# Optimization experiments

Measured on AMD Instinct MI355X. Metric: run time of the kernel, lower is better.

Reference implementation:

```python
import jax, jax.numpy as jnp
import numpy as np

P, H_OUT, D, NX = 32, 1, 256, 16
S_A = -0.1

def layernorm(x, g, b, eps=1e-5):
    mu = jnp.mean(x, axis=-1, keepdims=True)
    var = jnp.var(x, axis=-1, keepdims=True)
    return (x - mu) * jax.lax.rsqrt(var + eps) * g + b

def setup_inputs() -> dict:
    key = jax.random.key(0)
    ks = jax.random.split(key, 16)
    B, L = 8, 2048
    y = jax.random.normal(ks[0], (B, L, P), jnp.float32)
    Win = jax.random.normal(ks[1], (P, D), jnp.float32) / np.sqrt(P)
    bin_ = jnp.zeros((D,), jnp.float32)
    ng = jnp.ones((D,), jnp.float32); nb = jnp.zeros((D,), jnp.float32)
    # A = -10*rand + s_A, with A[:,0] = s_A (fix first state of each channel)
    A = -10.0 * jax.random.uniform(ks[2], (D, NX), jnp.float32) + S_A
    A = A.at[:, 0].set(S_A)
    W_B = jax.random.normal(ks[3], (NX, D), jnp.float32)
    W_C = jax.random.normal(ks[4], (NX, D), jnp.float32)
    q_delta = jax.random.normal(ks[5], (D,), jnp.float32)
    p_delta = jax.random.normal(ks[6], (1,), jnp.float32)
    nfg = jnp.ones((D,), jnp.float32); nfb = jnp.zeros((D,), jnp.float32)
    W1 = jax.random.normal(ks[7], (D, D), jnp.float32) / np.sqrt(D)
    b1 = jnp.zeros((D,), jnp.float32)
    W2 = jax.random.normal(ks[8], (D, H_OUT * P), jnp.float32) / np.sqrt(D)
    b2 = jnp.zeros((H_OUT * P,), jnp.float32)
    return {"y": y, "Win": Win, "bin_": bin_, "ng": ng, "nb": nb, "A": A,
            "W_B": W_B, "W_C": W_C, "q_delta": q_delta, "p_delta": p_delta,
            "nfg": nfg, "nfb": nfb, "W1": W1, "b1": b1, "W2": W2, "b2": b2}

def selective_scan(u, delta, A, Bm, Cm):
    # u: (B,L,D), delta: (B,L), A: (D,NX), Bm/Cm: (B,L,NX)
    dA = jnp.exp(delta[..., None, None] * A)                      # (B,L,D,NX)
    dBu = delta[..., None, None] * Bm[:, :, None, :] * u[..., None]  # (B,L,D,NX)
    x0 = jnp.zeros((u.shape[0], u.shape[2], A.shape[1]), u.dtype)
    def step(x, inp):
        dA_t, dBu_t, C_t = inp
        x = dA_t * x + dBu_t                                      # (B,D,NX)
        y_t = jnp.einsum('bdn,bn->bd', x, C_t)
        return x, y_t
    _, ys = jax.lax.scan(step, x0, (dA.transpose(1, 0, 2, 3),
                                    dBu.transpose(1, 0, 2, 3),
                                    Cm.transpose(1, 0, 2)))
    return ys.transpose(1, 0, 2)                                  # (B,L,D)

def reference(y, Win, bin_, ng, nb, A, W_B, W_C, q_delta, p_delta,
              nfg, nfb, W1, b1, W2, b2):
    B, L, _ = y.shape
    h = y @ Win + bin_                                            # (B,L,D)
    hn = layernorm(h, ng, nb)
    delta = jax.nn.softplus(p_delta[0] + jnp.einsum('bld,d->bl', hn, q_delta))
    Bm = jnp.einsum('nd,bld->bln', W_B, hn)
    Cm = jnp.einsum('nd,bld->bln', W_C, hn)
    upd = selective_scan(hn, delta, A, Bm, Cm)
    h = h + upd
    h = layernorm(h, nfg, nfb)
    out = jax.nn.gelu(h @ W1 + b1, approximate=False) @ W2 + b2
    return out.reshape(B, L, H_OUT, P)
```

## Files before the change

### kernel.cpp

```cpp
#include <hip/hip_runtime.h>
#include <math.h>

#define D 256
#define NX 16
#define L 2048
#define NBATCH 8
#define NTOK (NBATCH * L)
#define CL 32
#define NCH (L / CL)
#define LOG2E 1.44269504088896340736f

typedef float f32x4 __attribute__((ext_vector_type(4)));
typedef short bf16x8 __attribute__((ext_vector_type(8)));

__device__ __forceinline__ unsigned short f2bf(float x) {
  unsigned u = __float_as_uint(x);
  u = u + 0x7fffu + ((u >> 16) & 1u);
  return (unsigned short)(u >> 16);
}
__device__ __forceinline__ float bf2f(unsigned short h) {
  return __uint_as_float(((unsigned)h) << 16);
}

__global__ __launch_bounds__(256) void k0_prep(const float* __restrict__ A,
                                               const float* __restrict__ WB,
                                               const float* __restrict__ WC,
                                               const float* __restrict__ W1,
                                               const float* __restrict__ W2,
                                               float* __restrict__ At,
                                               float* __restrict__ Wbct,
                                               unsigned short* __restrict__ W1fh,
                                               unsigned short* __restrict__ W1fl,
                                               unsigned short* __restrict__ W2fh,
                                               unsigned short* __restrict__ W2fl) {
  int i = blockIdx.x * 256 + threadIdx.x;
  if (i < 4096) {
    int d = i >> 4, n = i & 15;
    At[n * D + d] = A[i] * LOG2E;
  } else if (i < 12288) {
    int j = i - 4096;
    int d = j >> 5, c = j & 31;
    Wbct[j] = (c < 16) ? WB[c * D + d] : WC[(c - 16) * D + d];
  } else if (i < 77824) {
    int e = i - 12288;
    int j = e & 7, l = (e >> 3) & 63, tt = (e >> 9) & 15, s = e >> 13;
    int k = s * 32 + ((l >> 4) << 3) + j;
    int n = tt * 16 + (l & 15);
    float x = W1[k * 256 + n];
    unsigned short h = f2bf(x);
    W1fh[e] = h;
    W1fl[e] = f2bf(x - bf2f(h));
  } else {
    int e = i - 77824;
    int j = e & 7, l = (e >> 3) & 63, tt = (e >> 9) & 1, s = e >> 10;
    int k = s * 32 + ((l >> 4) << 3) + j;
    int n = tt * 16 + (l & 15);
    float x = W2[k * 32 + n];
    unsigned short h = f2bf(x);
    W2fh[e] = h;
    W2fl[e] = f2bf(x - bf2f(h));
  }
}

__global__ __launch_bounds__(256) void k1a_front_scan(
    const float* __restrict__ y, const float* __restrict__ Win,
    const float* __restrict__ bin_, const float* __restrict__ ng,
    const float* __restrict__ nb, const float* __restrict__ Wbct,
    const float* __restrict__ qd, const float* __restrict__ pd,
    const float* __restrict__ At,
    float* __restrict__ hn, float* __restrict__ delta,
    float* __restrict__ Bm, float* __restrict__ Cm,
    float* __restrict__ muv, float* __restrict__ irsv,
    float* __restrict__ EX, float* __restrict__ T) {
  __shared__ float sy[32][32];
  __shared__ float sh[32][260];
  __shared__ float sB[32][NX];
  __shared__ float sdelta[32];
  int t = threadIdx.x;
  int tok0 = blockIdx.x * 32;
  {
    const float4* src = (const float4*)(y + (size_t)tok0 * 32);
    ((float4*)sy)[t] = src[t];
  }
  __syncthreads();
  int dcol = t & 63;
  int jrow = t >> 6;
  int d4 = dcol * 4;
  float4 bv = ((const float4*)bin_)[dcol];
  float4 acc[8];
  #pragma unroll
  for (int jj = 0; jj < 8; ++jj) acc[jj] = bv;
  const float4* Win4 = (const float4*)Win;
  #pragma unroll
  for (int k = 0; k < 32; ++k) {
    float4 wv = Win4[k * 64 + dcol];
    #pragma unroll
    for (int jj = 0; jj < 8; ++jj) {
      float av = sy[jrow * 8 + jj][k];
      acc[jj].x = fmaf(av, wv.x, acc[jj].x);
      acc[jj].y = fmaf(av, wv.y, acc[jj].y);
      acc[jj].z = fmaf(av, wv.z, acc[jj].z);
      acc[jj].w = fmaf(av, wv.w, acc[jj].w);
    }
  }
  float4 g4 = ((const float4*)ng)[dcol];
  float4 nb4 = ((const float4*)nb)[dcol];
  float4 q4 = ((const float4*)qd)[dcol];
  float pd0 = pd[0];
  #pragma unroll
  for (int jj = 0; jj < 8; ++jj) {
    int j = jrow * 8 + jj;
    int tok = tok0 + j;
    float4 a = acc[jj];
    float s1 = a.x + a.y + a.z + a.w;
    float s2 = a.x * a.x + a.y * a.y + a.z * a.z + a.w * a.w;
    #pragma unroll
    for (int off = 1; off < 64; off <<= 1) {
      s1 += __shfl_xor(s1, off);
      s2 += __shfl_xor(s2, off);
    }
    float mu = s1 * (1.f / D);
    float var = s2 * (1.f / D) - mu * mu;
    float rstd = rsqrtf(var + 1e-5f);
    if (dcol == 0) { muv[tok] = mu; irsv[tok] = sqrtf(var + 1e-5f); }
    float4 v4;
    v4.x = (a.x - mu) * rstd * g4.x + nb4.x;
    v4.y = (a.y - mu) * rstd * g4.y + nb4.y;
    v4.z = (a.z - mu) * rstd * g4.z + nb4.z;
    v4.w = (a.w - mu) * rstd * g4.w + nb4.w;
    ((float4*)(hn + (size_t)tok * D))[dcol] = v4;
    *(float4*)&sh[j][d4] = v4;
    float dd = v4.x * q4.x + v4.y * q4.y + v4.z * q4.z + v4.w * q4.w;
    #pragma unroll
    for (int off = 1; off < 64; off <<= 1) dd += __shfl_xor(dd, off);
    if (dcol == 0) {
      float xx = pd0 + dd;
      float dv = (xx > 20.f) ? xx : log1pf(expf(xx));
      delta[tok] = dv;
      sdelta[j] = dv;
    }
  }
  __syncthreads();
  if (t < 32) {
    float v = sdelta[t];
    #pragma unroll
    for (int off = 1; off < 32; off <<= 1) v += __shfl_xor(v, off);
    if (t == 0) T[blockIdx.x] = v;
  }
  int col4 = t & 7;
  int j = t >> 3;
  const float4* W4 = (const float4*)Wbct;
  float4 o = make_float4(0.f, 0.f, 0.f, 0.f);
  #pragma unroll 8
  for (int d = 0; d < 256; ++d) {
    float av = sh[j][d];
    float4 w = W4[d * 8 + col4];
    o.x = fmaf(av, w.x, o.x);
    o.y = fmaf(av, w.y, o.y);
    o.z = fmaf(av, w.z, o.z);
    o.w = fmaf(av, w.w, o.w);
  }
  int tokj = tok0 + j;
  if (col4 < 4) {
    ((float4*)(Bm + (size_t)tokj * NX))[col4] = o;
    *(float4*)&sB[j][col4 * 4] = o;
  } else {
    ((float4*)(Cm + (size_t)tokj * NX))[col4 - 4] = o;
  }
  __syncthreads();
  float a16[16];
  #pragma unroll
  for (int n = 0; n < 16; ++n) a16[n] = At[n * D + t];
  float x16[16];
  #pragma unroll
  for (int n = 0; n < 16; ++n) x16[n] = 0.f;
  for (int lo = 0; lo < CL; ++lo) {
    float dlt = sdelta[lo];
    float du = dlt * sh[lo][t];
    #pragma unroll
    for (int n = 0; n < 16; ++n)
      x16[n] = fmaf(exp2f(dlt * a16[n]), x16[n], du * sB[lo][n]);
  }
  size_t exbase = (size_t)blockIdx.x * (NX * D) + t;
  #pragma unroll
  for (int n = 0; n < 16; ++n) EX[exbase + n * D] = x16[n];
}

__global__ __launch_bounds__(256) void k2b_chunkscan(
    const float* __restrict__ At, const float* __restrict__ T,
    float* __restrict__ EX) {
  __shared__ float sT[NCH];
  int b = blockIdx.x >> 4;
  int rem = ((blockIdx.x & 15) << 8) | threadIdx.x;
  if (threadIdx.x < NCH) sT[threadIdx.x] = T[b * NCH + threadIdx.x];
  __syncthreads();
  float A2 = At[rem];
  size_t base = ((size_t)b << 18) + rem;
  float eq[4];
  #pragma unroll
  for (int j = 0; j < 4; ++j) eq[j] = EX[base + ((size_t)j << 12)];
  float x = 0.f;
  #pragma unroll 4
  for (int c = 0; c < NCH; ++c) {
    float e = eq[c & 3];
    if (c + 4 < NCH) eq[c & 3] = EX[base + ((size_t)(c + 4) << 12)];
    EX[base + ((size_t)c << 12)] = x;
    x = fmaf(exp2f(sT[c] * A2), x, e);
  }
}

__device__ __forceinline__ float gelu_exact(float x) {
  return 0.5f * x * (1.f + erff(x * 0.70710678118654752440f));
}

__global__ __launch_bounds__(256) void k2cd_scan_mlp(
    const float* __restrict__ hn, const float* __restrict__ delta,
    const float* __restrict__ Bm, const float* __restrict__ Cm,
    const float* __restrict__ At, const float* __restrict__ EX,
    const float* __restrict__ muv, const float* __restrict__ irsv,
    const float* __restrict__ ng, const float* __restrict__ nb,
    const float* __restrict__ nfg, const float* __restrict__ nfb,
    const unsigned short* __restrict__ W1fh, const unsigned short* __restrict__ W1fl,
    const unsigned short* __restrict__ W2fh, const unsigned short* __restrict__ W2fl,
    const float* __restrict__ b1, const float* __restrict__ b2,
    float* __restrict__ out) {
  __shared__ float s_az[32 * 260];
  __shared__ __align__(16) unsigned short sAh[32 * 256];
  __shared__ __align__(16) unsigned short sAl[32 * 256];
  __shared__ float sB[32][NX];
  __shared__ float sC[32][NX];
  __shared__ float sdelta[32];
  __shared__ float smu[32];
  __shared__ float sirs[32];
  int t = threadIdx.x;
  int tok0 = blockIdx.x * 32;
  size_t tokbase = (size_t)tok0;
  if (t < 32) {
    sdelta[t] = delta[tokbase + t];
    smu[t] = muv[tokbase + t];
    sirs[t] = irsv[tokbase + t];
  }
  for (int i = t; i < 32 * NX; i += 256) {
    ((float*)sB)[i] = Bm[tokbase * NX + i];
    ((float*)sC)[i] = Cm[tokbase * NX + i];
  }
  float a16[16], x16[16];
  size_t exbase = (size_t)blockIdx.x * (NX * D) + t;
  #pragma unroll
  for (int n = 0; n < 16; ++n) {
    a16[n] = At[n * D + t];
    x16[n] = EX[exbase + n * D];
  }
  float nb_d = nb[t];
  float invg = 1.0f / ng[t];
  __syncthreads();
  for (int lo = 0; lo < CL; ++lo) {
    float hv = hn[(tokbase + lo) * D + t];
    float dlt = sdelta[lo];
    float du = dlt * hv;
    float p = 0.f;
    #pragma unroll
    for (int n = 0; n < 16; ++n) {
      x16[n] = fmaf(exp2f(dlt * a16[n]), x16[n], du * sB[lo][n]);
      p = fmaf(x16[n], sC[lo][n], p);
    }
    float h = fmaf((hv - nb_d) * invg, sirs[lo], smu[lo]);
    s_az[lo * 260 + t] = h + p;
  }
  __syncthreads();
  int dcol = t & 63, jrow = t >> 6;
  int d4 = dcol * 4, j8 = jrow * 8;
  {
    float4 g4 = ((const float4*)nfg)[dcol];
    float4 b4 = ((const float4*)nfb)[dcol];
    for (int jj = 0; jj < 8; ++jj) {
      int lo = j8 + jj;
      float4 v = *(float4*)&s_az[lo * 260 + d4];
      float s1 = v.x + v.y + v.z + v.w;
      float s2 = v.x * v.x + v.y * v.y + v.z * v.z + v.w * v.w;
      #pragma unroll
      for (int off = 1; off < 64; off <<= 1) {
        s1 += __shfl_xor(s1, off);
        s2 += __shfl_xor(s2, off);
      }
      float mu2 = s1 * (1.f / D);
      float var2 = s2 * (1.f / D) - mu2 * mu2;
      float rstd2 = rsqrtf(var2 + 1e-5f);
      float4 o;
      o.x = (v.x - mu2) * rstd2 * g4.x + b4.x;
      o.y = (v.y - mu2) * rstd2 * g4.y + b4.y;
      o.z = (v.z - mu2) * rstd2 * g4.z + b4.z;
      o.w = (v.w - mu2) * rstd2 * g4.w + b4.w;
      unsigned short h0 = f2bf(o.x), h1 = f2bf(o.y), h2 = f2bf(o.z), h3 = f2bf(o.w);
      unsigned short q0 = f2bf(o.x - bf2f(h0));
      unsigned short q1 = f2bf(o.y - bf2f(h1));
      unsigned short q2 = f2bf(o.z - bf2f(h2));
      unsigned short q3 = f2bf(o.w - bf2f(h3));
      unsigned off16 = ((unsigned)(d4 * 2)) ^ ((unsigned)(lo & 7) << 4);
      uint2 hv2, lv2;
      hv2.x = (unsigned)h0 | ((unsigned)h1 << 16);
      hv2.y = (unsigned)h2 | ((unsigned)h3 << 16);
      lv2.x = (unsigned)q0 | ((unsigned)q1 << 16);
      lv2.y = (unsigned)q2 | ((unsigned)q3 << 16);
      *(uint2*)((char*)sAh + lo * 512 + off16) = hv2;
      *(uint2*)((char*)sAl + lo * 512 + off16) = lv2;
    }
  }
  __syncthreads();
  int l = t & 63, w = t >> 6;
  const bf16x8* B1h = (const bf16x8*)W1fh;
  const bf16x8* B1l = (const bf16x8*)W1fl;
  f32x4 acc[2][4];
  #pragma unroll
  for (int m = 0; m < 2; ++m)
    #pragma unroll
    for (int n = 0; n < 4; ++n) {
      f32x4 z4 = {0.f, 0.f, 0.f, 0.f};
      acc[m][n] = z4;
    }
  #pragma unroll 2
  for (int s = 0; s < 8; ++s) {
    bf16x8 ah[2], al[2];
    #pragma unroll
    for (int m = 0; m < 2; ++m) {
      int row = m * 16 + (l & 15);
      unsigned off16 = ((unsigned)(s * 64 + ((l >> 4) << 4))) ^ ((unsigned)(row & 7) << 4);
      ah[m] = *(const bf16x8*)((const char*)sAh + row * 512 + off16);
      al[m] = *(const bf16x8*)((const char*)sAl + row * 512 + off16);
    }
    #pragma unroll
    for (int n = 0; n < 4; ++n) {
      int bi = (s * 16 + w * 4 + n) * 64 + l;
      bf16x8 bh = B1h[bi];
      bf16x8 bl = B1l[bi];
      #pragma unroll
      for (int m = 0; m < 2; ++m) {
        acc[m][n] = __builtin_amdgcn_mfma_f32_16x16x32_bf16(ah[m], bh, acc[m][n], 0, 0, 0);
        acc[m][n] = __builtin_amdgcn_mfma_f32_16x16x32_bf16(al[m], bh, acc[m][n], 0, 0, 0);
        acc[m][n] = __builtin_amdgcn_mfma_f32_16x16x32_bf16(ah[m], bl, acc[m][n], 0, 0, 0);
      }
    }
  }
  __syncthreads();
  #pragma unroll
  for (int n = 0; n < 4; ++n) {
    int colz = w * 64 + n * 16 + (l & 15);
    float b1v = b1[colz];
    #pragma unroll
    for (int m = 0; m < 2; ++m) {
      #pragma unroll
      for (int r = 0; r < 4; ++r) {
        int row = m * 16 + ((l >> 4) << 2) + r;
        float zv = gelu_exact(acc[m][n][r] + b1v);
        unsigned short zh = f2bf(zv);
        unsigned short zl = f2bf(zv - bf2f(zh));
        unsigned off16 = ((unsigned)(colz * 2)) ^ ((unsigned)(row & 7) << 4);
        *(unsigned short*)((char*)sAh + row * 512 + off16) = zh;
        *(unsigned short*)((char*)sAl + row * 512 + off16) = zl;
      }
    }
  }
  __syncthreads();
  int mw = w >> 1, nw = w & 1;
  const bf16x8* B2h = (const bf16x8*)W2fh;
  const bf16x8* B2l = (const bf16x8*)W2fl;
  f32x4 acc2 = {0.f, 0.f, 0.f, 0.f};
  #pragma unroll 2
  for (int s = 0; s < 8; ++s) {
    int row = mw * 16 + (l & 15);
    unsigned off16 = ((unsigned)(s * 64 + ((l >> 4) << 4))) ^ ((unsigned)(row & 7) << 4);
    bf16x8 zh8 = *(const bf16x8*)((const char*)sAh + row * 512 + off16);
    bf16x8 zl8 = *(const bf16x8*)((const char*)sAl + row * 512 + off16);
    int bi = (s * 2 + nw) * 64 + l;
    bf16x8 bh = B2h[bi];
    bf16x8 bl = B2l[bi];
    acc2 = __builtin_amdgcn_mfma_f32_16x16x32_bf16(zh8, bh, acc2, 0, 0, 0);
    acc2 = __builtin_amdgcn_mfma_f32_16x16x32_bf16(zl8, bh, acc2, 0, 0, 0);
    acc2 = __builtin_amdgcn_mfma_f32_16x16x32_bf16(zh8, bl, acc2, 0, 0, 0);
  }
  int colo = nw * 16 + (l & 15);
  float b2v = b2[colo];
  #pragma unroll
  for (int r = 0; r < 4; ++r) {
    int row = mw * 16 + ((l >> 4) << 2) + r;
    out[(size_t)(tok0 + row) * 32 + colo] = acc2[r] + b2v;
  }
}

extern "C" void kernel_launch(void* const* d_in, const int* in_sizes, int n_in,
                              void* d_out, int out_size, void* d_ws, size_t ws_size,
                              hipStream_t stream) {
  const float* y    = (const float*)d_in[0];
  const float* Win  = (const float*)d_in[1];
  const float* bin_ = (const float*)d_in[2];
  const float* ng   = (const float*)d_in[3];
  const float* nb   = (const float*)d_in[4];
  const float* A    = (const float*)d_in[5];
  const float* WB   = (const float*)d_in[6];
  const float* WC   = (const float*)d_in[7];
  const float* qd   = (const float*)d_in[8];
  const float* pd   = (const float*)d_in[9];
  const float* nfg  = (const float*)d_in[10];
  const float* nfb  = (const float*)d_in[11];
  const float* W1   = (const float*)d_in[12];
  const float* b1   = (const float*)d_in[13];
  const float* W2   = (const float*)d_in[14];
  const float* b2   = (const float*)d_in[15];

  float* ws = (float*)d_ws;
  float* hnbuf = ws;
  float* delta = ws + 4194304;
  float* Bm    = delta + NTOK;
  float* Cm    = Bm + NTOK * NX;
  float* muv   = Cm + NTOK * NX;
  float* irsv  = muv + NTOK;
  float* Tbuf  = irsv + NTOK;
  float* At    = Tbuf + NBATCH * NCH;
  float* Wbct  = At + D * NX;
  float* EX    = Wbct + D * 32;
  unsigned short* W1fh = (unsigned short*)(EX + 2097152);
  unsigned short* W1fl = W1fh + 65536;
  unsigned short* W2fh = W1fl + 65536;
  unsigned short* W2fl = W2fh + 8192;

  k0_prep<<<336, 256, 0, stream>>>(A, WB, WC, W1, W2, At, Wbct,
                                   W1fh, W1fl, W2fh, W2fl);
  k1a_front_scan<<<NTOK / 32, 256, 0, stream>>>(y, Win, bin_, ng, nb, Wbct,
                                                qd, pd, At, hnbuf, delta, Bm,
                                                Cm, muv, irsv, EX, Tbuf);
  k2b_chunkscan<<<NBATCH * 16, 256, 0, stream>>>(At, Tbuf, EX);
  k2cd_scan_mlp<<<NTOK / 32, 256, 0, stream>>>(hnbuf, delta, Bm, Cm, At, EX,
                                               muv, irsv, ng, nb, nfg, nfb,
                                               W1fh, W1fl, W2fh, W2fl,
                                               b1, b2, (float*)d_out);
}
```

Baseline: 218.5 us.

## Split front kernel from chunk scan, halve token tile, widen chunkscan grid, add lo*lo MFMA

Splits the fused front/scan kernel in two. The front kernel now uses 16-token blocks and computes the B/C projection as a split-K over two half-warps groups with a shared-memory reduction. A separate scan kernel reloads hn, Bm and delta to build the chunk states. The chunk-prefix kernel moves to 64-thread blocks with a 4x larger grid for more parallelism. The MLP MFMAs also gain a fourth lo*lo product term for accuracy, which adds tensor-core work and extra global traffic from the new kernel launch.

```diff
diff --git a/kernel.cpp b/kernel.cpp
--- a/kernel.cpp
+++ b/kernel.cpp
@@ -62,41 +62,36 @@
   }
 }
 
-__global__ __launch_bounds__(256) void k1a_front_scan(
+__global__ __launch_bounds__(256, 4) void k1a_front(
     const float* __restrict__ y, const float* __restrict__ Win,
     const float* __restrict__ bin_, const float* __restrict__ ng,
     const float* __restrict__ nb, const float* __restrict__ Wbct,
     const float* __restrict__ qd, const float* __restrict__ pd,
-    const float* __restrict__ At,
     float* __restrict__ hn, float* __restrict__ delta,
     float* __restrict__ Bm, float* __restrict__ Cm,
-    float* __restrict__ muv, float* __restrict__ irsv,
-    float* __restrict__ EX, float* __restrict__ T) {
-  __shared__ float sy[32][32];
-  __shared__ float sh[32][260];
-  __shared__ float sB[32][NX];
-  __shared__ float sdelta[32];
+    float* __restrict__ muv, float* __restrict__ irsv) {
+  __shared__ float sy[16][32];
+  __shared__ float sh[16][260];
+  __shared__ float sph[2 * 16 * 32];
   int t = threadIdx.x;
-  int tok0 = blockIdx.x * 32;
-  {
-    const float4* src = (const float4*)(y + (size_t)tok0 * 32);
-    ((float4*)sy)[t] = src[t];
-  }
+  int tok0 = blockIdx.x * 16;
+  if (t < 128)
+    ((float4*)sy)[t] = ((const float4*)(y + (size_t)tok0 * 32))[t];
   __syncthreads();
   int dcol = t & 63;
-  int jrow = t >> 6;
+  int w = t >> 6;
   int d4 = dcol * 4;
   float4 bv = ((const float4*)bin_)[dcol];
-  float4 acc[8];
-  #pragma unroll
-  for (int jj = 0; jj < 8; ++jj) acc[jj] = bv;
+  float4 acc[4];
+  #pragma unroll
+  for (int jj = 0; jj < 4; ++jj) acc[jj] = bv;
   const float4* Win4 = (const float4*)Win;
   #pragma unroll
   for (int k = 0; k < 32; ++k) {
     float4 wv = Win4[k * 64 + dcol];
     #pragma unroll
-    for (int jj = 0; jj < 8; ++jj) {
-      float av = sy[jrow * 8 + jj][k];
+    for (int jj = 0; jj < 4; ++jj) {
+      float av = sy[w * 4 + jj][k];
       acc[jj].x = fmaf(av, wv.x, acc[jj].x);
       acc[jj].y = fmaf(av, wv.y, acc[jj].y);
       acc[jj].z = fmaf(av, wv.z, acc[jj].z);
@@ -108,8 +103,8 @@
   float4 q4 = ((const float4*)qd)[dcol];
   float pd0 = pd[0];
   #pragma unroll
-  for (int jj = 0; jj < 8; ++jj) {
-    int j = jrow * 8 + jj;
+  for (int jj = 0; jj < 4; ++jj) {
+    int j = w * 4 + jj;
     int tok = tok0 + j;
     float4 a = acc[jj];
     float s1 = a.x + a.y + a.z + a.w;
@@ -135,11 +130,57 @@
     for (int off = 1; off < 64; off <<= 1) dd += __shfl_xor(dd, off);
     if (dcol == 0) {
       float xx = pd0 + dd;
-      float dv = (xx > 20.f) ? xx : log1pf(expf(xx));
-      delta[tok] = dv;
-      sdelta[j] = dv;
-    }
-  }
+      delta[tok] = (xx > 20.f) ? xx : log1pf(expf(xx));
+    }
+  }
+  __syncthreads();
+  int c4 = t & 7;
+  int jc = (t >> 3) & 15;
+  int hk = t >> 7;
+  const float* shrow = &sh[jc][hk * 128];
+  const float4* W4 = (const float4*)Wbct + (size_t)hk * 128 * 8;
+  float4 o = make_float4(0.f, 0.f, 0.f, 0.f);
+  #pragma unroll 8
+  for (int k = 0; k < 128; ++k) {
+    float av = shrow[k];
+    float4 wv = W4[k * 8 + c4];
+    o.x = fmaf(av, wv.x, o.x);
+    o.y = fmaf(av, wv.y, o.y);
+    o.z = fmaf(av, wv.z, o.z);
+    o.w = fmaf(av, wv.w, o.w);
+  }
+  *(float4*)&sph[(((hk << 4) | jc) << 5) + c4 * 4] = o;
+  __syncthreads();
+  if (t < 128) {
+    int j2 = t >> 3, cc = t & 7;
+    float4 r0 = *(float4*)&sph[(j2 << 5) + cc * 4];
+    float4 r1 = *(float4*)&sph[((16 + j2) << 5) + cc * 4];
+    float4 r;
+    r.x = r0.x + r1.x; r.y = r0.y + r1.y;
+    r.z = r0.z + r1.z; r.w = r0.w + r1.w;
+    int tokj = tok0 + j2;
+    if (cc < 4) ((float4*)(Bm + (size_t)tokj * NX))[cc] = r;
+    else        ((float4*)(Cm + (size_t)tokj * NX))[cc - 4] = r;
+  }
+}
+
+__global__ __launch_bounds__(256) void k1s_scan(
+    const float* __restrict__ hn, const float* __restrict__ delta,
+    const float* __restrict__ Bm, const float* __restrict__ At,
+    float* __restrict__ EX, float* __restrict__ T) {
+  __shared__ float sh[32][260];
+  __shared__ float sB[32][NX];
+  __shared__ float sdelta[32];
+  int t = threadIdx.x;
+  int tok0 = blockIdx.x * 32;
+  const float4* hn4 = (const float4*)(hn + (size_t)tok0 * D);
+  for (int i = t; i < 2048; i += 256) {
+    int row = i >> 6, c4 = i & 63;
+    *(float4*)&sh[row][c4 * 4] = hn4[i];
+  }
+  for (int i = t; i < 32 * NX; i += 256)
+    ((float*)sB)[i] = Bm[(size_t)tok0 * NX + i];
+  if (t < 32) sdelta[t] = delta[tok0 + t];
   __syncthreads();
   if (t < 32) {
     float v = sdelta[t];
@@ -147,27 +188,6 @@
     for (int off = 1; off < 32; off <<= 1) v += __shfl_xor(v, off);
     if (t == 0) T[blockIdx.x] = v;
   }
-  int col4 = t & 7;
-  int j = t >> 3;
-  const float4* W4 = (const float4*)Wbct;
-  float4 o = make_float4(0.f, 0.f, 0.f, 0.f);
-  #pragma unroll 8
-  for (int d = 0; d < 256; ++d) {
-    float av = sh[j][d];
-    float4 w = W4[d * 8 + col4];
-    o.x = fmaf(av, w.x, o.x);
-    o.y = fmaf(av, w.y, o.y);
-    o.z = fmaf(av, w.z, o.z);
-    o.w = fmaf(av, w.w, o.w);
-  }
-  int tokj = tok0 + j;
-  if (col4 < 4) {
-    ((float4*)(Bm + (size_t)tokj * NX))[col4] = o;
-    *(float4*)&sB[j][col4 * 4] = o;
-  } else {
-    ((float4*)(Cm + (size_t)tokj * NX))[col4 - 4] = o;
-  }
-  __syncthreads();
   float a16[16];
   #pragma unroll
   for (int n = 0; n < 16; ++n) a16[n] = At[n * D + t];
@@ -186,13 +206,13 @@
   for (int n = 0; n < 16; ++n) EX[exbase + n * D] = x16[n];
 }
 
-__global__ __launch_bounds__(256) void k2b_chunkscan(
+__global__ __launch_bounds__(64) void k2b_chunkscan(
     const float* __restrict__ At, const float* __restrict__ T,
     float* __restrict__ EX) {
   __shared__ float sT[NCH];
-  int b = blockIdx.x >> 4;
-  int rem = ((blockIdx.x & 15) << 8) | threadIdx.x;
-  if (threadIdx.x < NCH) sT[threadIdx.x] = T[b * NCH + threadIdx.x];
+  int b = blockIdx.x >> 6;
+  int rem = ((blockIdx.x & 63) << 6) | threadIdx.x;
+  sT[threadIdx.x] = T[b * NCH + threadIdx.x];
   __syncthreads();
   float A2 = At[rem];
   size_t base = ((size_t)b << 18) + rem;
@@ -338,6 +358,7 @@
         acc[m][n] = __builtin_amdgcn_mfma_f32_16x16x32_bf16(ah[m], bh, acc[m][n], 0, 0, 0);
         acc[m][n] = __builtin_amdgcn_mfma_f32_16x16x32_bf16(al[m], bh, acc[m][n], 0, 0, 0);
         acc[m][n] = __builtin_amdgcn_mfma_f32_16x16x32_bf16(ah[m], bl, acc[m][n], 0, 0, 0);
+        acc[m][n] = __builtin_amdgcn_mfma_f32_16x16x32_bf16(al[m], bl, acc[m][n], 0, 0, 0);
       }
     }
   }
@@ -377,6 +398,7 @@
     acc2 = __builtin_amdgcn_mfma_f32_16x16x32_bf16(zh8, bh, acc2, 0, 0, 0);
     acc2 = __builtin_amdgcn_mfma_f32_16x16x32_bf16(zl8, bh, acc2, 0, 0, 0);
     acc2 = __builtin_amdgcn_mfma_f32_16x16x32_bf16(zh8, bl, acc2, 0, 0, 0);
+    acc2 = __builtin_amdgcn_mfma_f32_16x16x32_bf16(zl8, bl, acc2, 0, 0, 0);
   }
   int colo = nw * 16 + (l & 15);
   float b2v = b2[colo];
@@ -425,10 +447,11 @@
 
   k0_prep<<<336, 256, 0, stream>>>(A, WB, WC, W1, W2, At, Wbct,
                                    W1fh, W1fl, W2fh, W2fl);
-  k1a_front_scan<<<NTOK / 32, 256, 0, stream>>>(y, Win, bin_, ng, nb, Wbct,
-                                                qd, pd, At, hnbuf, delta, Bm,
-                                                Cm, muv, irsv, EX, Tbuf);
-  k2b_chunkscan<<<NBATCH * 16, 256, 0, stream>>>(At, Tbuf, EX);
+  k1a_front<<<NTOK / 16, 256, 0, stream>>>(y, Win, bin_, ng, nb, Wbct,
+                                           qd, pd, hnbuf, delta, Bm, Cm,
+                                           muv, irsv);
+  k1s_scan<<<NTOK / 32, 256, 0, stream>>>(hnbuf, delta, Bm, At, EX, Tbuf);
+  k2b_chunkscan<<<NBATCH * 64, 64, 0, stream>>>(At, Tbuf, EX);
   k2cd_scan_mlp<<<NTOK / 32, 256, 0, stream>>>(hnbuf, delta, Bm, Cm, At, EX,
                                                muv, irsv, ng, nb, nfg, nfb,
                                                W1fh, W1fl, W2fh, W2fl,
```

Result: slower. 291.2 us (+33.3%).

## Cut front-kernel register pressure, widen chunk-scan grid, add fourth split-bf16 MFMA term

Applied to the files above, without the earlier changes.

The front kernel now computes its input projection in groups of two tokens rather than holding eight float4 accumulators, and declares launch bounds with a minimum of 4 blocks per multiprocessor, so it needs fewer registers and can keep more waves resident. The chunk-scan kernel is relaunched with 64-thread blocks and four times as many blocks, giving more parallelism across the GPU. The MLP MFMA loops gain a lo×lo product term, which improves precision at the cost of a third more matrix instructions. The grouped loop also reloads the Win weights four times instead of once.

```diff
diff --git a/kernel.cpp b/kernel.cpp
--- a/kernel.cpp
+++ b/kernel.cpp
@@ -62,7 +62,7 @@
   }
 }
 
-__global__ __launch_bounds__(256) void k1a_front_scan(
+__global__ __launch_bounds__(256, 4) void k1a_front_scan(
     const float* __restrict__ y, const float* __restrict__ Win,
     const float* __restrict__ bin_, const float* __restrict__ ng,
     const float* __restrict__ nb, const float* __restrict__ Wbct,
@@ -87,57 +87,56 @@
   int jrow = t >> 6;
   int d4 = dcol * 4;
   float4 bv = ((const float4*)bin_)[dcol];
-  float4 acc[8];
-  #pragma unroll
-  for (int jj = 0; jj < 8; ++jj) acc[jj] = bv;
-  const float4* Win4 = (const float4*)Win;
-  #pragma unroll
-  for (int k = 0; k < 32; ++k) {
-    float4 wv = Win4[k * 64 + dcol];
-    #pragma unroll
-    for (int jj = 0; jj < 8; ++jj) {
-      float av = sy[jrow * 8 + jj][k];
-      acc[jj].x = fmaf(av, wv.x, acc[jj].x);
-      acc[jj].y = fmaf(av, wv.y, acc[jj].y);
-      acc[jj].z = fmaf(av, wv.z, acc[jj].z);
-      acc[jj].w = fmaf(av, wv.w, acc[jj].w);
-    }
-  }
   float4 g4 = ((const float4*)ng)[dcol];
   float4 nb4 = ((const float4*)nb)[dcol];
   float4 q4 = ((const float4*)qd)[dcol];
   float pd0 = pd[0];
-  #pragma unroll
-  for (int jj = 0; jj < 8; ++jj) {
-    int j = jrow * 8 + jj;
-    int tok = tok0 + j;
-    float4 a = acc[jj];
-    float s1 = a.x + a.y + a.z + a.w;
-    float s2 = a.x * a.x + a.y * a.y + a.z * a.z + a.w * a.w;
-    #pragma unroll
-    for (int off = 1; off < 64; off <<= 1) {
-      s1 += __shfl_xor(s1, off);
-      s2 += __shfl_xor(s2, off);
-    }
-    float mu = s1 * (1.f / D);
-    float var = s2 * (1.f / D) - mu * mu;
-    float rstd = rsqrtf(var + 1e-5f);
-    if (dcol == 0) { muv[tok] = mu; irsv[tok] = sqrtf(var + 1e-5f); }
-    float4 v4;
-    v4.x = (a.x - mu) * rstd * g4.x + nb4.x;
-    v4.y = (a.y - mu) * rstd * g4.y + nb4.y;
-    v4.z = (a.z - mu) * rstd * g4.z + nb4.z;
-    v4.w = (a.w - mu) * rstd * g4.w + nb4.w;
-    ((float4*)(hn + (size_t)tok * D))[dcol] = v4;
-    *(float4*)&sh[j][d4] = v4;
-    float dd = v4.x * q4.x + v4.y * q4.y + v4.z * q4.z + v4.w * q4.w;
-    #pragma unroll
-    for (int off = 1; off < 64; off <<= 1) dd += __shfl_xor(dd, off);
-    if (dcol == 0) {
-      float xx = pd0 + dd;
-      float dv = (xx > 20.f) ? xx : log1pf(expf(xx));
-      delta[tok] = dv;
-      sdelta[j] = dv;
+  const float4* Win4 = (const float4*)Win;
+  for (int g = 0; g < 4; ++g) {
+    int j0 = jrow * 8 + g * 2;
+    float4 acc0 = bv, acc1 = bv;
+    #pragma unroll 4
+    for (int k = 0; k < 32; ++k) {
+      float4 wv = Win4[k * 64 + dcol];
+      float a0 = sy[j0][k];
+      float a1 = sy[j0 + 1][k];
+      acc0.x = fmaf(a0, wv.x, acc0.x); acc1.x = fmaf(a1, wv.x, acc1.x);
+      acc0.y = fmaf(a0, wv.y, acc0.y); acc1.y = fmaf(a1, wv.y, acc1.y);
+      acc0.z = fmaf(a0, wv.z, acc0.z); acc1.z = fmaf(a1, wv.z, acc1.z);
+      acc0.w = fmaf(a0, wv.w, acc0.w); acc1.w = fmaf(a1, wv.w, acc1.w);
+    }
+    #pragma unroll
+    for (int p = 0; p < 2; ++p) {
+      int j = j0 + p;
+      int tok = tok0 + j;
+      float4 a = (p == 0) ? acc0 : acc1;
+      float s1 = a.x + a.y + a.z + a.w;
+      float s2 = a.x * a.x + a.y * a.y + a.z * a.z + a.w * a.w;
+      #pragma unroll
+      for (int off = 1; off < 64; off <<= 1) {
+        s1 += __shfl_xor(s1, off);
+        s2 += __shfl_xor(s2, off);
+      }
+      float mu = s1 * (1.f / D);
+      float var = s2 * (1.f / D) - mu * mu;
+      float rstd = rsqrtf(var + 1e-5f);
+      if (dcol == 0) { muv[tok] = mu; irsv[tok] = sqrtf(var + 1e-5f); }
+      float4 v4;
+      v4.x = (a.x - mu) * rstd * g4.x + nb4.x;
+      v4.y = (a.y - mu) * rstd * g4.y + nb4.y;
+      v4.z = (a.z - mu) * rstd * g4.z + nb4.z;
+      v4.w = (a.w - mu) * rstd * g4.w + nb4.w;
+      ((float4*)(hn + (size_t)tok * D))[dcol] = v4;
+      *(float4*)&sh[j][d4] = v4;
+      float dd = v4.x * q4.x + v4.y * q4.y + v4.z * q4.z + v4.w * q4.w;
+      #pragma unroll
+      for (int off = 1; off < 64; off <<= 1) dd += __shfl_xor(dd, off);
+      if (dcol == 0) {
+        float xx = pd0 + dd;
+        float dv = (xx > 20.f) ? xx : log1pf(expf(xx));
+        delta[tok] = dv;
+        sdelta[j] = dv;
+      }
     }
   }
   __syncthreads();
@@ -151,7 +150,7 @@
   int j = t >> 3;
   const float4* W4 = (const float4*)Wbct;
   float4 o = make_float4(0.f, 0.f, 0.f, 0.f);
-  #pragma unroll 8
+  #pragma unroll 4
   for (int d = 0; d < 256; ++d) {
     float av = sh[j][d];
     float4 w = W4[d * 8 + col4];
@@ -186,13 +185,13 @@
   for (int n = 0; n < 16; ++n) EX[exbase + n * D] = x16[n];
 }
 
-__global__ __launch_bounds__(256) void k2b_chunkscan(
+__global__ __launch_bounds__(64) void k2b_chunkscan(
     const float* __restrict__ At, const float* __restrict__ T,
     float* __restrict__ EX) {
   __shared__ float sT[NCH];
-  int b = blockIdx.x >> 4;
-  int rem = ((blockIdx.x & 15) << 8) | threadIdx.x;
-  if (threadIdx.x < NCH) sT[threadIdx.x] = T[b * NCH + threadIdx.x];
+  int b = blockIdx.x >> 6;
+  int rem = ((blockIdx.x & 63) << 6) | threadIdx.x;
+  sT[threadIdx.x] = T[b * NCH + threadIdx.x];
   __syncthreads();
   float A2 = At[rem];
   size_t base = ((size_t)b << 18) + rem;
@@ -338,6 +337,7 @@
         acc[m][n] = __builtin_amdgcn_mfma_f32_16x16x32_bf16(ah[m], bh, acc[m][n], 0, 0, 0);
         acc[m][n] = __builtin_amdgcn_mfma_f32_16x16x32_bf16(al[m], bh, acc[m][n], 0, 0, 0);
         acc[m][n] = __builtin_amdgcn_mfma_f32_16x16x32_bf16(ah[m], bl, acc[m][n], 0, 0, 0);
+        acc[m][n] = __builtin_amdgcn_mfma_f32_16x16x32_bf16(al[m], bl, acc[m][n], 0, 0, 0);
       }
     }
   }
@@ -377,6 +377,7 @@
     acc2 = __builtin_amdgcn_mfma_f32_16x16x32_bf16(zh8, bh, acc2, 0, 0, 0);
     acc2 = __builtin_amdgcn_mfma_f32_16x16x32_bf16(zl8, bh, acc2, 0, 0, 0);
     acc2 = __builtin_amdgcn_mfma_f32_16x16x32_bf16(zh8, bl, acc2, 0, 0, 0);
+    acc2 = __builtin_amdgcn_mfma_f32_16x16x32_bf16(zl8, bl, acc2, 0, 0, 0);
   }
   int colo = nw * 16 + (l & 15);
   float b2v = b2[colo];
@@ -428,7 +429,7 @@
   k1a_front_scan<<<NTOK / 32, 256, 0, stream>>>(y, Win, bin_, ng, nb, Wbct,
                                                 qd, pd, At, hnbuf, delta, Bm,
                                                 Cm, muv, irsv, EX, Tbuf);
-  k2b_chunkscan<<<NBATCH * 16, 256, 0, stream>>>(At, Tbuf, EX);
+  k2b_chunkscan<<<NBATCH * 64, 64, 0, stream>>>(At, Tbuf, EX);
   k2cd_scan_mlp<<<NTOK / 32, 256, 0, stream>>>(hnbuf, delta, Bm, Cm, At, EX,
                                                muv, irsv, ng, nb, nfg, nfb,
                                                W1fh, W1fl, W2fh, W2fl,
```

Result: faster. 210.2 us (-3.8%).
